# Kernel optimization log

Hardware: AMD Instinct MI355X
Metric: run time of the kernel (lower is better)

Reference implementation:

```python
import jax, jax.numpy as jnp
import numpy as np
from jax import lax

V, E, HE, HD, B, T, DEC_STEPS = 50000, 300, 512, 1024, 64, 400, 80


def gru_cell(x, h, w_ih, w_hh, b_ih, b_hh):
    # PyTorch GRU cell semantics
    gi = x @ w_ih.T + b_ih          # [B, 3H]
    gh = h @ w_hh.T + b_hh          # [B, 3H]
    ir, iz, in_ = jnp.split(gi, 3, axis=-1)
    hr, hz, hn = jnp.split(gh, 3, axis=-1)
    r = jax.nn.sigmoid(ir + hr)
    z = jax.nn.sigmoid(iz + hz)
    n = jnp.tanh(in_ + r * hn)
    return (1.0 - z) * n + z * h


def setup_inputs() -> dict:
    key = jax.random.key(0)
    ks = jax.random.split(key, 20)
    s = 0.05
    texts = jax.random.randint(ks[0], (B, T), 0, V, dtype=jnp.int32)
    text_length = jax.random.randint(ks[1], (B,), 1, T + 1, dtype=jnp.int32)
    emb = jax.random.normal(ks[2], (V, E), jnp.float32) * s
    def w(k, shape):
        return jax.random.normal(k, shape, jnp.float32) * s
    return {
        "texts": texts,
        "text_length": text_length,
        "emb": emb,
        "enc_wih_f": w(ks[3], (3 * HE, E)),
        "enc_whh_f": w(ks[4], (3 * HE, HE)),
        "enc_bih_f": w(ks[5], (3 * HE,)),
        "enc_bhh_f": w(ks[6], (3 * HE,)),
        "enc_wih_b": w(ks[7], (3 * HE, E)),
        "enc_whh_b": w(ks[8], (3 * HE, HE)),
        "enc_bih_b": w(ks[9], (3 * HE,)),
        "enc_bhh_b": w(ks[10], (3 * HE,)),
        "dec_wih": w(ks[11], (3 * HD, E)),
        "dec_whh": w(ks[12], (3 * HD, HD)),
        "dec_bih": w(ks[13], (3 * HD,)),
        "dec_bhh": w(ks[14], (3 * HD,)),
        "out_w": w(ks[15], (V, HD)),
        "out_b": w(ks[16], (V,)),
    }


def reference(texts, text_length, emb,
              enc_wih_f, enc_whh_f, enc_bih_f, enc_bhh_f,
              enc_wih_b, enc_whh_b, enc_bih_b, enc_bhh_b,
              dec_wih, dec_whh, dec_bih, dec_bhh,
              out_w, out_b):
    b, t = texts.shape
    embed = emb[texts]                      # [B,T,E] (dropout is identity in eval)
    xs = jnp.swapaxes(embed, 0, 1)          # [T,B,E]
    lens = text_length[:, None]             # [B,1]
    h0 = jnp.zeros((b, HE), emb.dtype)

    # forward direction: final hidden = state at last valid timestep (pack semantics)
    def fstep(h, inp):
        x, tt = inp
        hn = gru_cell(x, h, enc_wih_f, enc_whh_f, enc_bih_f, enc_bhh_f)
        return jnp.where(tt < lens, hn, h), None
    hf, _ = lax.scan(fstep, h0, (xs, jnp.arange(t)))

    # backward direction: processes x[len-1] ... x[0]; skip padded positions
    def bstep(h, inp):
        x, tt = inp
        hn = gru_cell(x, h, enc_wih_b, enc_whh_b, enc_bih_b, enc_bhh_b)
        return jnp.where(tt < lens, hn, h), None
    hb, _ = lax.scan(bstep, h0, (xs[::-1], jnp.arange(t)[::-1]))

    hidden = jnp.concatenate([hf, hb], axis=-1)   # [B, 1024]

    sos = jnp.ones((b,), jnp.int32)               # inputs = ones
    def dstep(carry, _):
        h, tok = carry
        x = emb[tok]                              # [B,E]
        h = gru_cell(x, h, dec_wih, dec_whh, dec_bih, dec_bhh)
        logits = h @ out_w.T + out_b              # [B,V]
        tok = jnp.argmax(logits, axis=-1).astype(jnp.int32)
        return (h, tok), tok
    _, toks = lax.scan(dstep, (hidden, sos), None, length=DEC_STEPS)  # [80,B]

    return jnp.swapaxes(toks, 0, 1).astype(jnp.float32)[:, :, None]  # [B,80,1]
```

## Files before the change

kernel.cpp:

```cpp
#include <hip/hip_runtime.h>
#include <stdint.h>

typedef unsigned int u32;
typedef unsigned long long u64;
typedef unsigned short u16;
typedef __attribute__((ext_vector_type(8))) short s8;
typedef __attribute__((ext_vector_type(4))) float f4;

#define NWG 256
#define TPB 512
#define NB 64
#define TT 400
#define EE 300
#define HEN 512
#define HD 1024
#define VV 50000
#define DEC 80
#define NTL 3125
#define NTLP 3136
#define LCAP 512
#define EOFF 39168
#define LGOFF 131072
#define LGSZ (LGOFF + 256)
#define RESC 0.00837f


struct P {
  const int* texts; const int* len; const float* emb;
  const float* ewih0; const float* ewhh0; const float* ebih0; const float* ebhh0;
  const float* ewih1; const float* ewhh1; const float* ebih1; const float* ebhh1;
  const float* dwih; const float* dwhh; const float* dbih; const float* dbhh;
  const float* outw; const float* outb;
  float* out;
  u16* owbf; float* xT; float* hTf; float* hTb; float* hTd; u16* hbf;
  u64* prt; int* tok; float* wn;
};

__device__ __forceinline__ u32 fkey(float v) {
  u32 u = __float_as_uint(v);
  return (u & 0x80000000u) ? ~u : (u | 0x80000000u);
}
__device__ __forceinline__ u16 f2bf(float f) {
  u32 u = __float_as_uint(f);
  u32 r = u + 0x7FFFu + ((u >> 16) & 1u);
  return (u16)(r >> 16);
}
__device__ __forceinline__ float sigm(float x) { return 1.f / (1.f + expf(-x)); }

__device__ __forceinline__ void gru_combine_epi(
    float* pb, const f4& ar, const f4& az, const f4& ax, const f4& ah,
    int jjb, int HL, const float* bih, const float* bhh,
    const float* hc, float* ho, int mask_t, const int* lenp, u16* hbf_out)
{
  const int tid = threadIdx.x, lane = tid & 63, wv = tid >> 6;
  const int wl = wv & 3;
  if (wv < 4) {
    #pragma unroll
    for (int j = 0; j < 4; j++) {
      pb[((wl * 16 + j * 4 + 0) * 64) + lane] = ar[j];
      pb[((wl * 16 + j * 4 + 1) * 64) + lane] = az[j];
      pb[((wl * 16 + j * 4 + 2) * 64) + lane] = ax[j];
      pb[((wl * 16 + j * 4 + 3) * 64) + lane] = ah[j];
    }
  }
  __syncthreads();
  if (wv >= 4) {
    #pragma unroll
    for (int j = 0; j < 4; j++) {
      pb[((wl * 16 + j * 4 + 0) * 64) + lane] += ar[j];
      pb[((wl * 16 + j * 4 + 1) * 64) + lane] += az[j];
      pb[((wl * 16 + j * 4 + 2) * 64) + lane] += ax[j];
      pb[((wl * 16 + j * 4 + 3) * 64) + lane] += ah[j];
    }
  }
  __syncthreads();
  if (tid < 256) {
    int b = tid & 63, j = tid >> 6;
    int jj = jjb + j;
    float r = 0, z = 0, xn = 0, hn = 0;
    #pragma unroll
    for (int w = 0; w < 4; w++) {
      int base = ((w * 16 + j * 4) * 64) + b;
      r  += pb[base];
      z  += pb[base + 64];
      xn += pb[base + 128];
      hn += pb[base + 192];
    }
    r = sigm(r + bih[jj] + bhh[jj]);
    z = sigm(z + bih[HL + jj] + bhh[HL + jj]);
    float nn = tanhf(xn + bih[2 * HL + jj] + r * (hn + bhh[2 * HL + jj]));
    float hold = hc[(size_t)jj * NB + b];
    float hv = (1.f - z) * nn + z * hold;
    if (lenp && mask_t >= lenp[b]) hv = hold;
    ho[(size_t)jj * NB + b] = hv;
    if (hbf_out) hbf_out[(size_t)b * HD + jj] = f2bf(hv);
  }
}

__global__ void __launch_bounds__(TPB, 2) prep_kernel(P p) {
  const int wg = blockIdx.x, tid = threadIdx.x;
  const int lane = tid & 63, wv = tid >> 6;
  const int gtid = wg * TPB + tid;
  int gwv = wg * 8 + wv;
  for (int v = gwv; v < VV; v += 2048) {
    const float* wr = p.outw + (size_t)v * HD + lane * 16;
    u16* dst = p.owbf + (size_t)v * HD + lane * 16;
    float sa = 0.f;
    u32 pk[8];
    #pragma unroll
    for (int q = 0; q < 4; q++) {
      float4 f = *(const float4*)(wr + q * 4);
      sa += f.x * f.x + f.y * f.y + f.z * f.z + f.w * f.w;
      pk[q * 2 + 0] = (u32)f2bf(f.x) | ((u32)f2bf(f.y) << 16);
      pk[q * 2 + 1] = (u32)f2bf(f.z) | ((u32)f2bf(f.w) << 16);
    }
    *(uint4*)(dst)     = make_uint4(pk[0], pk[1], pk[2], pk[3]);
    *(uint4*)(dst + 8) = make_uint4(pk[4], pk[5], pk[6], pk[7]);
    #pragma unroll
    for (int d = 1; d < 64; d <<= 1) sa += __shfl_xor(sa, d);
    if (lane == 0) p.wn[v] = sqrtf(sa);
  }
  const long long tot = (long long)TT * NB * EE;
  for (long long i = gtid; i < tot; i += (long long)NWG * TPB) {
    int t = (int)(i / (NB * EE));
    int rr = (int)(i % (NB * EE));
    int b2 = rr / EE, k = rr % EE;
    float v = p.emb[(size_t)p.texts[b2 * TT + t] * EE + k];
    p.xT[((size_t)t * EE + k) * NB + b2] = v;
  }
}

__global__ void __launch_bounds__(TPB, 1) enc_step_kernel(P p, int t) {
  __shared__ __align__(16) char smem[EOFF + 16384];
  const int wg = blockIdx.x, tid = threadIdx.x;
  const int lane = tid & 63, wv = tid >> 6;
  const int dir = wg >> 7;
  const int ejjb = (wg & 127) * 4;

  {
    const float* wih = dir ? p.ewih1 : p.ewih0;
    const float* whh = dir ? p.ewhh1 : p.ewhh0;
    float* lw = (float*)smem;
    for (int c = wv; c < 12; c += 8) {
      int g = c >> 2, j = c & 3;
      const float* sx = wih + (size_t)(g * HEN + ejjb + j) * EE;
      for (int k = lane; k < EE; k += 64) lw[k * 12 + c] = sx[k];
      const float* sh = whh + (size_t)(g * HEN + ejjb + j) * HEN;
      for (int k = lane; k < HEN; k += 64) lw[(EE + k) * 12 + c] = sh[k];
    }
  }
  __syncthreads();

  const float* bih = dir ? p.ebih1 : p.ebih0;
  const float* bhh = dir ? p.ebhh1 : p.ebhh0;
  float* hbase = dir ? p.hTb : p.hTf;
  const int te = dir ? (TT - 1 - t) : t;
  const float* hc = hbase + (size_t)(t & 1) * HEN * NB;
  float* ho = hbase + (size_t)((t + 1) & 1) * HEN * NB;
  const float* xsrc = p.xT + (size_t)te * EE * NB;

  const float* lw = (const float*)smem;
  const int KT = EE + HEN;
  const int vs = (wv * KT) >> 3, ve = ((wv + 1) * KT) >> 3;
  f4 ar = {0,0,0,0}, az = {0,0,0,0}, ax = {0,0,0,0}, ah = {0,0,0,0};
  const int xe = ve < EE ? ve : EE;
  int k = vs;
  for (; k + 8 <= xe; k += 8) {
    float xv[8];
    #pragma unroll
    for (int u = 0; u < 8; u++) xv[u] = xsrc[(size_t)(k + u) * NB + lane];
    #pragma unroll
    for (int u = 0; u < 8; u++) {
      const float* wp = lw + (k + u) * 12;
      f4 w0 = *(const f4*)wp; f4 w1 = *(const f4*)(wp + 4); f4 w2 = *(const f4*)(wp + 8);
      ar += xv[u] * w0; az += xv[u] * w1; ax += xv[u] * w2;
    }
  }
  for (; k < xe; k++) {
    float xv = xsrc[(size_t)k * NB + lane];
    const float* wp = lw + k * 12;
    f4 w0 = *(const f4*)wp; f4 w1 = *(const f4*)(wp + 4); f4 w2 = *(const f4*)(wp + 8);
    ar += xv * w0; az += xv * w1; ax += xv * w2;
  }
  k = vs > EE ? vs : EE;
  for (; k + 8 <= ve; k += 8) {
    float hv[8];
    #pragma unroll
    for (int u = 0; u < 8; u++) hv[u] = hc[(size_t)(k + u - EE) * NB + lane];
    #pragma unroll
    for (int u = 0; u < 8; u++) {
      const float* wp = lw + (k + u) * 12;
      f4 w0 = *(const f4*)wp; f4 w1 = *(const f4*)(wp + 4); f4 w2 = *(const f4*)(wp + 8);
      ar += hv[u] * w0; az += hv[u] * w1; ah += hv[u] * w2;
    }
  }
  for (; k < ve; k++) {
    float hv = hc[(size_t)(k - EE) * NB + lane];
    const float* wp = lw + k * 12;
    f4 w0 = *(const f4*)wp; f4 w1 = *(const f4*)(wp + 4); f4 w2 = *(const f4*)(wp + 8);
    ar += hv * w0; az += hv * w1; ah += hv * w2;
  }
  gru_combine_epi((float*)(smem + EOFF), ar, az, ax, ah, ejjb, HEN,
                  bih, bhh, hc, ho, te, p.len, nullptr);
}

__global__ void enc_join_kernel(P p) {
  int g = blockIdx.x * blockDim.x + threadIdx.x;
  int stride = gridDim.x * blockDim.x;
  for (int i = g; i < HD * NB; i += stride) {
    int k = i / NB, b2 = i % NB;
    float v = (k < HEN) ? p.hTf[(size_t)k * NB + b2]
                        : p.hTb[(size_t)(k - HEN) * NB + b2];
    p.hTd[i] = v;
  }
  if (g < NB) p.tok[g] = 1;
}

__global__ void __launch_bounds__(TPB, 1) dec_gru_kernel(P p, int s) {
  __shared__ __align__(16) float pb[4096];
  const int wg = blockIdx.x, tid = threadIdx.x;
  const int lane = tid & 63, wv = tid >> 6;
  const int jjb = wg * 4;
  const float* hc = p.hTd + (size_t)(s & 1) * HD * NB;
  float* ho = p.hTd + (size_t)((s + 1) & 1) * HD * NB;
  const float* wih = p.dwih; const float* whh = p.dwhh;
  const int KT = EE + HD;
  const int vs = (wv * KT) >> 3, ve = ((wv + 1) * KT) >> 3;
  f4 ar = {0,0,0,0}, az = {0,0,0,0}, ax = {0,0,0,0}, ah = {0,0,0,0};
  const int xe = ve < EE ? ve : EE;
  if (vs < EE) {
    const float* xr = p.emb + (size_t)p.tok[lane] * EE;
    int k = vs;
    for (; k + 4 <= xe; k += 4) {
      float xv[4];
      #pragma unroll
      for (int u = 0; u < 4; u++) xv[u] = xr[k + u];
      #pragma unroll
      for (int u = 0; u < 4; u++) {
        #pragma unroll
        for (int j = 0; j < 4; j++) {
          int jj = jjb + j;
          ar[j] = fmaf(xv[u], wih[(size_t)jj * EE + k + u], ar[j]);
          az[j] = fmaf(xv[u], wih[(size_t)(HD + jj) * EE + k + u], az[j]);
          ax[j] = fmaf(xv[u], wih[(size_t)(2 * HD + jj) * EE + k + u], ax[j]);
        }
      }
    }
    for (; k < xe; k++) {
      float xv = xr[k];
      #pragma unroll
      for (int j = 0; j < 4; j++) {
        int jj = jjb + j;
        ar[j] = fmaf(xv, wih[(size_t)jj * EE + k], ar[j]);
        az[j] = fmaf(xv, wih[(size_t)(HD + jj) * EE + k], az[j]);
        ax[j] = fmaf(xv, wih[(size_t)(2 * HD + jj) * EE + k], ax[j]);
      }
    }
  }
  int hs = vs - EE; if (hs < 0) hs = 0;
  const int he = ve - EE;
  int k = hs;
  for (; k + 4 <= he; k += 4) {
    float hv[4];
    #pragma unroll
    for (int u = 0; u < 4; u++) hv[u] = hc[(size_t)(k + u) * NB + lane];
    #pragma unroll
    for (int u = 0; u < 4; u++) {
      #pragma unroll
      for (int j = 0; j < 4; j++) {
        int jj = jjb + j;
        ar[j] = fmaf(hv[u], whh[(size_t)jj * HD + k + u], ar[j]);
        az[j] = fmaf(hv[u], whh[(size_t)(HD + jj) * HD + k + u], az[j]);
        ah[j] = fmaf(hv[u], whh[(size_t)(2 * HD + jj) * HD + k + u], ah[j]);
      }
    }
  }
  for (; k < he; k++) {
    float hv = hc[(size_t)k * NB + lane];
    #pragma unroll
    for (int j = 0; j < 4; j++) {
      int jj = jjb + j;
      ar[j] = fmaf(hv, whh[(size_t)jj * HD + k], ar[j]);
      az[j] = fmaf(hv, whh[(size_t)(HD + jj) * HD + k], az[j]);
      ah[j] = fmaf(hv, whh[(size_t)(2 * HD + jj) * HD + k], ah[j]);
    }
  }
  gru_combine_epi(pb, ar, az, ax, ah, jjb, HD, p.dbih, p.dbhh,
                  hc, ho, -1, nullptr, p.hbf);
}

__global__ void __launch_bounds__(TPB, 1) dec_logits_kernel(P p) {
  extern __shared__ __align__(16) char smem[];
  const int wg = blockIdx.x, tid = threadIdx.x;
  const int lane = tid & 63, wv = tid >> 6;
  u16* hA = (u16*)smem;
  float* hsq = (float*)(smem + LGOFF);
  const int l15 = lane & 15, quad = lane >> 4;
  const int gw = wg * 8 + wv;
  const bool two = (gw + 2048) < NTL;
  if (tid < 64) hsq[tid] = 0.f;
  __syncthreads();
  for (int i = tid; i < 8192; i += TPB) {
    int r = i >> 7, c = i & 127;
    uint4 q = *(const uint4*)(p.hbf + (size_t)r * HD + c * 8);
    *(uint4*)(hA + (size_t)r * 1024 + ((c ^ (r & 7)) * 8)) = q;
    u32 uu[4] = {q.x, q.y, q.z, q.w};
    float sq = 0.f;
    #pragma unroll
    for (int t2 = 0; t2 < 4; t2++) {
      float lo = __uint_as_float(uu[t2] << 16);
      float hi = __uint_as_float(uu[t2] & 0xffff0000u);
      sq = fmaf(lo, lo, fmaf(hi, hi, sq));
    }
    atomicAdd(&hsq[r], sq);
  }
  __syncthreads();
  f4 acc0[4], acc1[4];
  #pragma unroll
  for (int m = 0; m < 4; m++) {
    #pragma unroll
    for (int r = 0; r < 4; r++) { acc0[m][r] = 0.f; acc1[m][r] = 0.f; }
  }
  const u16* bp0 = p.owbf + (size_t)(gw * 16 + l15) * HD + quad * 8;
  const u16* bp1 = bp0 + (size_t)2048 * 16 * HD;
  const int x7 = l15 & 7;
  const u16* hrow = hA + l15 * 1024;
  #pragma unroll 4
  for (int kc = 0; kc < 32; kc++) {
    int ci = ((kc * 4 + quad) ^ x7) * 8;
    s8 b0 = *(const s8*)(bp0 + kc * 32);
    s8 a0 = *(const s8*)(hrow + ci);
    s8 a1 = *(const s8*)(hrow + 16384 + ci);
    s8 a2 = *(const s8*)(hrow + 32768 + ci);
    s8 a3 = *(const s8*)(hrow + 49152 + ci);
    acc0[0] = __builtin_amdgcn_mfma_f32_16x16x32_bf16(a0, b0, acc0[0], 0, 0, 0);
    acc0[1] = __builtin_amdgcn_mfma_f32_16x16x32_bf16(a1, b0, acc0[1], 0, 0, 0);
    acc0[2] = __builtin_amdgcn_mfma_f32_16x16x32_bf16(a2, b0, acc0[2], 0, 0, 0);
    acc0[3] = __builtin_amdgcn_mfma_f32_16x16x32_bf16(a3, b0, acc0[3], 0, 0, 0);
    if (two) {
      s8 b1 = *(const s8*)(bp1 + kc * 32);
      acc1[0] = __builtin_amdgcn_mfma_f32_16x16x32_bf16(a0, b1, acc1[0], 0, 0, 0);
      acc1[1] = __builtin_amdgcn_mfma_f32_16x16x32_bf16(a1, b1, acc1[1], 0, 0, 0);
      acc1[2] = __builtin_amdgcn_mfma_f32_16x16x32_bf16(a2, b1, acc1[2], 0, 0, 0);
      acc1[3] = __builtin_amdgcn_mfma_f32_16x16x32_bf16(a3, b1, acc1[3], 0, 0, 0);
    }
  }
  float hroot[4][4];
  #pragma unroll
  for (int m = 0; m < 4; m++)
    #pragma unroll
    for (int r = 0; r < 4; r++)
      hroot[m][r] = sqrtf(hsq[m * 16 + quad * 4 + r]);
  auto epi = [&](int nt, f4* acc) {
    int col = nt * 16 + l15;
    float bias = p.outb[col];
    float wnc = p.wn[col];
    #pragma unroll
    for (int m = 0; m < 4; m++) {
      #pragma unroll
      for (int r = 0; r < 4; r++) {
        float v = acc[m][r] + bias;
        float e = RESC * hroot[m][r] * wnc + 1e-5f;
        u32 klo = fkey(v - e), kup = fkey(v + e);
        #pragma unroll
        for (int d = 1; d < 16; d <<= 1) {
          u32 ol = __shfl_xor(klo, d); if (ol > klo) klo = ol;
          u32 ou = __shfl_xor(kup, d); if (ou > kup) kup = ou;
        }
        if (l15 == 0)
          p.prt[(size_t)(m * 16 + quad * 4 + r) * NTLP + nt] =
              ((u64)klo << 32) | kup;
      }
    }
  };
  epi(gw, acc0);
  if (two) epi(gw + 2048, acc1);
}

__global__ void __launch_bounds__(TPB, 1) dec_rescue_kernel(P p, int s) {
  __shared__ float hb[HD];
  __shared__ u64 red[8];
  __shared__ u64 gmp, bestp;
  __shared__ int ncp;
  __shared__ int list[LCAP];
  const int b = blockIdx.x, tid = threadIdx.x;
  const int lane = tid & 63, wv = tid >> 6;
  const float* ho = p.hTd + (size_t)((s + 1) & 1) * HD * NB;
  for (int i = tid; i < HD; i += TPB) hb[i] = ho[(size_t)i * NB + b];
  if (tid == 0) { bestp = 0ull; ncp = 0; }
  __syncthreads();
  u64 pv[7];
  u64 mx = 0;
  #pragma unroll
  for (int i = 0; i < 7; i++) {
    int nt = tid + i * TPB;
    pv[i] = (nt < NTL) ? p.prt[(size_t)b * NTLP + nt] : 0ull;
    if (pv[i] > mx) mx = pv[i];
  }
  #pragma unroll
  for (int d = 1; d < 64; d <<= 1) { u64 o = __shfl_xor(mx, d); if (o > mx) mx = o; }
  if (lane == 0) red[wv] = mx;
  __syncthreads();
  if (tid == 0) {
    u64 g = red[0];
    for (int w2 = 1; w2 < 8; w2++) if (red[w2] > g) g = red[w2];
    gmp = g;
  }
  __syncthreads();
  const u32 thr = (u32)(gmp >> 32);
  #pragma unroll
  for (int i = 0; i < 7; i++) {
    if ((u32)pv[i] >= thr) {
      int ix = atomicAdd(&ncp, 1);
      if (ix < LCAP) list[ix] = tid + i * TPB;
    }
  }
  __syncthreads();
  int total = ncp;
  int nc = total < LCAP ? total : LCAP;
  const int c16 = tid >> 5, seg = tid & 31;
  u64 lb = 0;
  auto rescue = [&](int nt) {
    int v = nt * 16 + c16;
    const float* wr = p.outw + (size_t)v * HD;
    float sm = 0.f;
    #pragma unroll 8
    for (int i = 0; i < 32; i++) {
      int k = seg + 32 * i;
      sm = fmaf(hb[k], wr[k], sm);
    }
    #pragma unroll
    for (int d = 1; d < 32; d <<= 1) sm += __shfl_xor(sm, d);
    if (seg == 0) {
      float lg = sm + p.outb[v];
      u64 k2 = ((u64)fkey(lg) << 32) | (~(u32)v);
      if (k2 > lb) lb = k2;
    }
  };
  for (int ci = 0; ci < nc; ci++) rescue(list[ci]);
  if (total > LCAP) {
    for (int nt = 0; nt < NTL; nt++)
      if ((u32)p.prt[(size_t)b * NTLP + nt] >= thr) rescue(nt);
  }
  if (seg == 0 && lb) atomicMax((unsigned long long*)&bestp, lb);
  __syncthreads();
  if (tid == 0) {
    u32 v = ~(u32)(bestp);
    p.tok[b] = (int)v;
    p.out[b * DEC + s] = (float)v;
  }
}

__global__ void seq2seq_init(float* hTf, float* hTb) {
  int g = blockIdx.x * blockDim.x + threadIdx.x;
  int n = 2 * HEN * NB;
  for (int i = g; i < n; i += gridDim.x * blockDim.x) { hTf[i] = 0.f; hTb[i] = 0.f; }
}

extern "C" void kernel_launch(void* const* d_in, const int* in_sizes, int n_in,
                              void* d_out, int out_size, void* d_ws, size_t ws_size,
                              hipStream_t stream) {
  char* w = (char*)d_ws;
  size_t off = 0;
  auto carve = [&](size_t n) {
    void* q = w + off;
    off = (off + n + 255) & ~(size_t)255;
    return q;
  };
  P p;
  p.texts = (const int*)d_in[0];
  p.len   = (const int*)d_in[1];
  p.emb   = (const float*)d_in[2];
  p.ewih0 = (const float*)d_in[3];  p.ewhh0 = (const float*)d_in[4];
  p.ebih0 = (const float*)d_in[5];  p.ebhh0 = (const float*)d_in[6];
  p.ewih1 = (const float*)d_in[7];  p.ewhh1 = (const float*)d_in[8];
  p.ebih1 = (const float*)d_in[9];  p.ebhh1 = (const float*)d_in[10];
  p.dwih  = (const float*)d_in[11]; p.dwhh  = (const float*)d_in[12];
  p.dbih  = (const float*)d_in[13]; p.dbhh  = (const float*)d_in[14];
  p.outw  = (const float*)d_in[15]; p.outb  = (const float*)d_in[16];
  p.out   = (float*)d_out;
  p.owbf  = (u16*)carve((size_t)VV * HD * 2);
  p.xT    = (float*)carve((size_t)TT * EE * NB * 4);
  p.hTf   = (float*)carve((size_t)2 * HEN * NB * 4);
  p.hTb   = (float*)carve((size_t)2 * HEN * NB * 4);
  p.hTd   = (float*)carve((size_t)2 * HD * NB * 4);
  p.hbf   = (u16*)carve((size_t)NB * HD * 2);
  p.prt   = (u64*)carve((size_t)NB * NTLP * 8);
  p.tok   = (int*)carve(256);
  p.wn    = (float*)carve((size_t)VV * 4);
  if (off > ws_size) return;

  hipFuncSetAttribute((const void*)dec_logits_kernel,
                      hipFuncAttributeMaxDynamicSharedMemorySize, LGSZ);

  seq2seq_init<<<dim3(64), dim3(256), 0, stream>>>(p.hTf, p.hTb);
  prep_kernel<<<dim3(NWG), dim3(TPB), 0, stream>>>(p);
  for (int t = 0; t < TT; t++)
    enc_step_kernel<<<dim3(NWG), dim3(TPB), 0, stream>>>(p, t);
  enc_join_kernel<<<dim3(64), dim3(256), 0, stream>>>(p);
  for (int s = 0; s < DEC; s++) {
    dec_gru_kernel<<<dim3(NWG), dim3(TPB), 0, stream>>>(p, s);
    dec_logits_kernel<<<dim3(NWG), dim3(TPB), LGSZ, stream>>>(p);
    dec_rescue_kernel<<<dim3(NB), dim3(TPB), 0, stream>>>(p, s);
  }
}
```

Before: 14.70 ms.

## Replace per-step kernel launches with persistent cooperative kernels and grid barriers

Runs the 400 encoder steps and 80 decoder steps inside two persistent cooperative kernels, separated by a hierarchical atomic grid barrier, in place of about 640 separate launches. Encoder weights are staged into LDS once per block and no longer reloaded every step. Hidden states are kept as full per-step histories, so no double-buffer hazards arise across the barrier, and they are accessed with relaxed agent-scope atomics. The aim is to remove launch overhead and repeated weight staging. The cost is spin-barrier latency and a larger workspace, with a fallback to the launch-per-step path when the workspace is too small.

Result: slower. 16.79 ms (+14.3%).

```diff
diff --git a/kernel.cpp b/kernel.cpp
--- a/kernel.cpp
+++ b/kernel.cpp
@@ -21,8 +21,16 @@
 #define LCAP 512
 #define EOFF 39168
 #define LGOFF 131072
-#define LGSZ (LGOFF + 256)
+#define DSZ (LGOFF + 16384)
 #define RESC 0.00837f
+
+#define BD_GRP   0
+#define BD_ROOT  1024
+#define BD_EPO   1152
+#define BX_GRP   1280
+#define BX_ROOT  2304
+#define BX_EPO   2368
+#define BAR_WORDS 2432
 
 
 struct P {
@@ -32,9 +40,50 @@
   const float* dwih; const float* dwhh; const float* dbih; const float* dbhh;
   const float* outw; const float* outb;
   float* out;
-  u16* owbf; float* xT; float* hTf; float* hTb; float* hTd; u16* hbf;
-  u64* prt; int* tok; float* wn;
+  u16* owbf; float* xT; u64* prt; int* tok; float* wn; u32* bar;
+  float* hrF; float* hrB;
+  float* hTdR;
+  u16* hbfR;
+  float* hTf; float* hTb; float* hTd; u16* hbf;
 };
+
+__device__ __forceinline__ float cld(const float* a) {
+  return __hip_atomic_load(const_cast<float*>(a), __ATOMIC_RELAXED, __HIP_MEMORY_SCOPE_AGENT);
+}
+__device__ __forceinline__ void cst(float* a, float v) {
+  __hip_atomic_store(a, v, __ATOMIC_RELAXED, __HIP_MEMORY_SCOPE_AGENT);
+}
+__device__ __forceinline__ u64 cld(const u64* a) {
+  return __hip_atomic_load(const_cast<u64*>(a), __ATOMIC_RELAXED, __HIP_MEMORY_SCOPE_AGENT);
+}
+__device__ __forceinline__ void cst(u64* a, u64 v) {
+  __hip_atomic_store(a, v, __ATOMIC_RELAXED, __HIP_MEMORY_SCOPE_AGENT);
+}
+__device__ __forceinline__ int cld(const int* a) {
+  return __hip_atomic_load(const_cast<int*>(a), __ATOMIC_RELAXED, __HIP_MEMORY_SCOPE_AGENT);
+}
+__device__ __forceinline__ void cst(int* a, int v) {
+  __hip_atomic_store(a, v, __ATOMIC_RELAXED, __HIP_MEMORY_SCOPE_AGENT);
+}
+__device__ __forceinline__ void cst(u16* a, u16 v) {
+  __hip_atomic_store(a, v, __ATOMIC_RELAXED, __HIP_MEMORY_SCOPE_AGENT);
+}
+
+__device__ __forceinline__ void gbarx(u32* grp, u32* root, u32* epo,
+                                      u32 e, u32 gsz, u32 nroot) {
+  __syncthreads();
+  if (threadIdx.x == 0) {
+    u32 old = __hip_atomic_fetch_add(grp, 1u, __ATOMIC_RELAXED, __HIP_MEMORY_SCOPE_AGENT);
+    if (old == e * gsz + (gsz - 1u)) {
+      u32 r = __hip_atomic_fetch_add(root, 1u, __ATOMIC_RELAXED, __HIP_MEMORY_SCOPE_AGENT);
+      if (r == e * nroot + (nroot - 1u))
+        __hip_atomic_store(epo, e + 1u, __ATOMIC_RELAXED, __HIP_MEMORY_SCOPE_AGENT);
+    }
+    while (__hip_atomic_load(epo, __ATOMIC_RELAXED, __HIP_MEMORY_SCOPE_AGENT) < e + 1u)
+      __builtin_amdgcn_s_sleep(8);
+  }
+  __syncthreads();
+}
 
 __device__ __forceinline__ u32 fkey(float v) {
   u32 u = __float_as_uint(v);
@@ -47,6 +96,7 @@
 }
 __device__ __forceinline__ float sigm(float x) { return 1.f / (1.f + expf(-x)); }
 
+template<bool COH>
 __device__ __forceinline__ void gru_combine_epi(
     float* pb, const f4& ar, const f4& az, const f4& ax, const f4& ah,
     int jjb, int HL, const float* bih, const float* bhh,
@@ -92,73 +142,22 @@
     float hold = hc[(size_t)jj * NB + b];
     float hv = (1.f - z) * nn + z * hold;
     if (lenp && mask_t >= lenp[b]) hv = hold;
-    ho[(size_t)jj * NB + b] = hv;
-    if (hbf_out) hbf_out[(size_t)b * HD + jj] = f2bf(hv);
-  }
-}
-
-__global__ void __launch_bounds__(TPB, 2) prep_kernel(P p) {
-  const int wg = blockIdx.x, tid = threadIdx.x;
-  const int lane = tid & 63, wv = tid >> 6;
-  const int gtid = wg * TPB + tid;
-  int gwv = wg * 8 + wv;
-  for (int v = gwv; v < VV; v += 2048) {
-    const float* wr = p.outw + (size_t)v * HD + lane * 16;
-    u16* dst = p.owbf + (size_t)v * HD + lane * 16;
-    float sa = 0.f;
-    u32 pk[8];
-    #pragma unroll
-    for (int q = 0; q < 4; q++) {
-      float4 f = *(const float4*)(wr + q * 4);
-      sa += f.x * f.x + f.y * f.y + f.z * f.z + f.w * f.w;
-      pk[q * 2 + 0] = (u32)f2bf(f.x) | ((u32)f2bf(f.y) << 16);
-      pk[q * 2 + 1] = (u32)f2bf(f.z) | ((u32)f2bf(f.w) << 16);
-    }
-    *(uint4*)(dst)     = make_uint4(pk[0], pk[1], pk[2], pk[3]);
-    *(uint4*)(dst + 8) = make_uint4(pk[4], pk[5], pk[6], pk[7]);
-    #pragma unroll
-    for (int d = 1; d < 64; d <<= 1) sa += __shfl_xor(sa, d);
-    if (lane == 0) p.wn[v] = sqrtf(sa);
-  }
-  const long long tot = (long long)TT * NB * EE;
-  for (long long i = gtid; i < tot; i += (long long)NWG * TPB) {
-    int t = (int)(i / (NB * EE));
-    int rr = (int)(i % (NB * EE));
-    int b2 = rr / EE, k = rr % EE;
-    float v = p.emb[(size_t)p.texts[b2 * TT + t] * EE + k];
-    p.xT[((size_t)t * EE + k) * NB + b2] = v;
-  }
-}
-
-__global__ void __launch_bounds__(TPB, 1) enc_step_kernel(P p, int t) {
-  __shared__ __align__(16) char smem[EOFF + 16384];
-  const int wg = blockIdx.x, tid = threadIdx.x;
-  const int lane = tid & 63, wv = tid >> 6;
-  const int dir = wg >> 7;
-  const int ejjb = (wg & 127) * 4;
-
-  {
-    const float* wih = dir ? p.ewih1 : p.ewih0;
-    const float* whh = dir ? p.ewhh1 : p.ewhh0;
-    float* lw = (float*)smem;
-    for (int c = wv; c < 12; c += 8) {
-      int g = c >> 2, j = c & 3;
-      const float* sx = wih + (size_t)(g * HEN + ejjb + j) * EE;
-      for (int k = lane; k < EE; k += 64) lw[k * 12 + c] = sx[k];
-      const float* sh = whh + (size_t)(g * HEN + ejjb + j) * HEN;
-      for (int k = lane; k < HEN; k += 64) lw[(EE + k) * 12 + c] = sh[k];
-    }
-  }
-  __syncthreads();
-
-  const float* bih = dir ? p.ebih1 : p.ebih0;
-  const float* bhh = dir ? p.ebhh1 : p.ebhh0;
-  float* hbase = dir ? p.hTb : p.hTf;
-  const int te = dir ? (TT - 1 - t) : t;
-  const float* hc = hbase + (size_t)(t & 1) * HEN * NB;
-  float* ho = hbase + (size_t)((t + 1) & 1) * HEN * NB;
-  const float* xsrc = p.xT + (size_t)te * EE * NB;
-
+    if (COH) cst(ho + (size_t)jj * NB + b, hv);
+    else     ho[(size_t)jj * NB + b] = hv;
+    if (hbf_out) {
+      if (COH) cst(hbf_out + (size_t)b * HD + jj, f2bf(hv));
+      else     hbf_out[(size_t)b * HD + jj] = f2bf(hv);
+    }
+  }
+}
+
+template<bool COH>
+__device__ __forceinline__ void enc_step_body(
+    char* smem, int jjb, const float* xsrc,
+    const float* bih, const float* bhh,
+    const float* __restrict__ hc, float* ho, int te, const int* lenp)
+{
+  const int tid = threadIdx.x, lane = tid & 63, wv = tid >> 6;
   const float* lw = (const float*)smem;
   const int KT = EE + HEN;
   const int vs = (wv * KT) >> 3, ve = ((wv + 1) * KT) >> 3;
@@ -200,36 +199,39 @@
     f4 w0 = *(const f4*)wp; f4 w1 = *(const f4*)(wp + 4); f4 w2 = *(const f4*)(wp + 8);
     ar += hv * w0; az += hv * w1; ah += hv * w2;
   }
-  gru_combine_epi((float*)(smem + EOFF), ar, az, ax, ah, ejjb, HEN,
-                  bih, bhh, hc, ho, te, p.len, nullptr);
-}
-
-__global__ void enc_join_kernel(P p) {
-  int g = blockIdx.x * blockDim.x + threadIdx.x;
-  int stride = gridDim.x * blockDim.x;
-  for (int i = g; i < HD * NB; i += stride) {
-    int k = i / NB, b2 = i % NB;
-    float v = (k < HEN) ? p.hTf[(size_t)k * NB + b2]
-                        : p.hTb[(size_t)(k - HEN) * NB + b2];
-    p.hTd[i] = v;
-  }
-  if (g < NB) p.tok[g] = 1;
-}
-
-__global__ void __launch_bounds__(TPB, 1) dec_gru_kernel(P p, int s) {
-  __shared__ __align__(16) float pb[4096];
-  const int wg = blockIdx.x, tid = threadIdx.x;
-  const int lane = tid & 63, wv = tid >> 6;
-  const int jjb = wg * 4;
-  const float* hc = p.hTd + (size_t)(s & 1) * HD * NB;
-  float* ho = p.hTd + (size_t)((s + 1) & 1) * HD * NB;
+  gru_combine_epi<COH>((float*)(smem + EOFF), ar, az, ax, ah, jjb, HEN,
+                       bih, bhh, hc, ho, te, lenp, nullptr);
+}
+
+__device__ __forceinline__ void enc_stage_weights(char* smem, int dir, int ejjb,
+                                                  const P& p) {
+  const int tid = threadIdx.x, lane = tid & 63, wv = tid >> 6;
+  const float* wih = dir ? p.ewih1 : p.ewih0;
+  const float* whh = dir ? p.ewhh1 : p.ewhh0;
+  float* lw = (float*)smem;
+  for (int c = wv; c < 12; c += 8) {
+    int g = c >> 2, j = c & 3;
+    const float* sx = wih + (size_t)(g * HEN + ejjb + j) * EE;
+    for (int k = lane; k < EE; k += 64) lw[k * 12 + c] = sx[k];
+    const float* sh = whh + (size_t)(g * HEN + ejjb + j) * HEN;
+    for (int k = lane; k < HEN; k += 64) lw[(EE + k) * 12 + c] = sh[k];
+  }
+}
+
+template<bool COH>
+__device__ __forceinline__ void dec_gru_body(
+    const P& p, float* pb, int jjb,
+    const float* __restrict__ hc, float* ho, u16* hbf_out)
+{
+  const int tid = threadIdx.x, lane = tid & 63, wv = tid >> 6;
   const float* wih = p.dwih; const float* whh = p.dwhh;
   const int KT = EE + HD;
   const int vs = (wv * KT) >> 3, ve = ((wv + 1) * KT) >> 3;
   f4 ar = {0,0,0,0}, az = {0,0,0,0}, ax = {0,0,0,0}, ah = {0,0,0,0};
   const int xe = ve < EE ? ve : EE;
   if (vs < EE) {
-    const float* xr = p.emb + (size_t)p.tok[lane] * EE;
+    int tk = COH ? cld(p.tok + lane) : p.tok[lane];
+    const float* xr = p.emb + (size_t)tk * EE;
     int k = vs;
     for (; k + 4 <= xe; k += 4) {
       float xv[4];
@@ -285,12 +287,13 @@
       ah[j] = fmaf(hv, whh[(size_t)(2 * HD + jj) * HD + k], ah[j]);
     }
   }
-  gru_combine_epi(pb, ar, az, ax, ah, jjb, HD, p.dbih, p.dbhh,
-                  hc, ho, -1, nullptr, p.hbf);
-}
-
-__global__ void __launch_bounds__(TPB, 1) dec_logits_kernel(P p) {
-  extern __shared__ __align__(16) char smem[];
+  gru_combine_epi<COH>(pb, ar, az, ax, ah, jjb, HD, p.dbih, p.dbhh,
+                       hc, ho, -1, nullptr, hbf_out);
+}
+
+template<bool COH>
+__device__ __forceinline__ void dec_logits_body(const P& p, char* smem,
+                                                const u16* hbf_src) {
   const int wg = blockIdx.x, tid = threadIdx.x;
   const int lane = tid & 63, wv = tid >> 6;
   u16* hA = (u16*)smem;
@@ -302,7 +305,7 @@
   __syncthreads();
   for (int i = tid; i < 8192; i += TPB) {
     int r = i >> 7, c = i & 127;
-    uint4 q = *(const uint4*)(p.hbf + (size_t)r * HD + c * 8);
+    uint4 q = *(const uint4*)(hbf_src + (size_t)r * HD + c * 8);
     *(uint4*)(hA + (size_t)r * 1024 + ((c ^ (r & 7)) * 8)) = q;
     u32 uu[4] = {q.x, q.y, q.z, q.w};
     float sq = 0.f;
@@ -367,9 +370,11 @@
           u32 ol = __shfl_xor(klo, d); if (ol > klo) klo = ol;
           u32 ou = __shfl_xor(kup, d); if (ou > kup) kup = ou;
         }
-        if (l15 == 0)
-          p.prt[(size_t)(m * 16 + quad * 4 + r) * NTLP + nt] =
-              ((u64)klo << 32) | kup;
+        if (l15 == 0) {
+          u64 key = ((u64)klo << 32) | kup;
+          u64* dst = p.prt + (size_t)(m * 16 + quad * 4 + r) * NTLP + nt;
+          if (COH) cst(dst, key); else *dst = key;
+        }
       }
     }
   };
@@ -377,24 +382,31 @@
   if (two) epi(gw + 2048, acc1);
 }
 
-__global__ void __launch_bounds__(TPB, 1) dec_rescue_kernel(P p, int s) {
-  __shared__ float hb[HD];
-  __shared__ u64 red[8];
-  __shared__ u64 gmp, bestp;
-  __shared__ int ncp;
-  __shared__ int list[LCAP];
-  const int b = blockIdx.x, tid = threadIdx.x;
+template<bool COH>
+__device__ __forceinline__ void dec_rescue_body(const P& p, char* smem,
+                                                const float* ho, int s, int b) {
+  const int tid = threadIdx.x;
   const int lane = tid & 63, wv = tid >> 6;
-  const float* ho = p.hTd + (size_t)((s + 1) & 1) * HD * NB;
+  char* ms = smem + LGOFF;
+  float* hb = (float*)ms;
+  u64* red = (u64*)(ms + 4096);
+  u64* gmp = (u64*)(ms + 4160);
+  u64* bestp = (u64*)(ms + 4168);
+  int* ncp = (int*)(ms + 4176);
+  int* list = (int*)(ms + 4192);
   for (int i = tid; i < HD; i += TPB) hb[i] = ho[(size_t)i * NB + b];
-  if (tid == 0) { bestp = 0ull; ncp = 0; }
+  if (tid == 0) { *bestp = 0ull; *ncp = 0; }
   __syncthreads();
   u64 pv[7];
   u64 mx = 0;
   #pragma unroll
   for (int i = 0; i < 7; i++) {
     int nt = tid + i * TPB;
-    pv[i] = (nt < NTL) ? p.prt[(size_t)b * NTLP + nt] : 0ull;
+    pv[i] = 0ull;
+    if (nt < NTL) {
+      const u64* src = p.prt + (size_t)b * NTLP + nt;
+      pv[i] = COH ? cld(src) : *src;
+    }
     if (pv[i] > mx) mx = pv[i];
   }
   #pragma unroll
@@ -404,19 +416,19 @@
   if (tid == 0) {
     u64 g = red[0];
     for (int w2 = 1; w2 < 8; w2++) if (red[w2] > g) g = red[w2];
-    gmp = g;
-  }
-  __syncthreads();
-  const u32 thr = (u32)(gmp >> 32);
+    *gmp = g;
+  }
+  __syncthreads();
+  const u32 thr = (u32)(*gmp >> 32);
   #pragma unroll
   for (int i = 0; i < 7; i++) {
     if ((u32)pv[i] >= thr) {
-      int ix = atomicAdd(&ncp, 1);
+      int ix = atomicAdd(ncp, 1);
       if (ix < LCAP) list[ix] = tid + i * TPB;
     }
   }
   __syncthreads();
-  int total = ncp;
+  int total = *ncp;
   int nc = total < LCAP ? total : LCAP;
   const int c16 = tid >> 5, seg = tid & 31;
   u64 lb = 0;
@@ -439,22 +451,154 @@
   };
   for (int ci = 0; ci < nc; ci++) rescue(list[ci]);
   if (total > LCAP) {
-    for (int nt = 0; nt < NTL; nt++)
-      if ((u32)p.prt[(size_t)b * NTLP + nt] >= thr) rescue(nt);
-  }
-  if (seg == 0 && lb) atomicMax((unsigned long long*)&bestp, lb);
+    for (int nt = 0; nt < NTL; nt++) {
+      const u64* src = p.prt + (size_t)b * NTLP + nt;
+      u64 v = COH ? cld(src) : *src;
+      if ((u32)v >= thr) rescue(nt);
+    }
+  }
+  if (seg == 0 && lb) atomicMax((unsigned long long*)bestp, lb);
   __syncthreads();
   if (tid == 0) {
-    u32 v = ~(u32)(bestp);
-    p.tok[b] = (int)v;
+    u32 v = ~(u32)(*bestp);
+    if (COH) cst(p.tok + b, (int)v); else p.tok[b] = (int)v;
     p.out[b * DEC + s] = (float)v;
   }
 }
 
-__global__ void seq2seq_init(float* hTf, float* hTb) {
+__global__ void __launch_bounds__(TPB, 2) prep_kernel(P p) {
+  const int wg = blockIdx.x, tid = threadIdx.x;
+  const int lane = tid & 63, wv = tid >> 6;
+  const int gtid = wg * TPB + tid;
+  int gwv = wg * 8 + wv;
+  for (int v = gwv; v < VV; v += 2048) {
+    const float* wr = p.outw + (size_t)v * HD + lane * 16;
+    u16* dst = p.owbf + (size_t)v * HD + lane * 16;
+    float sa = 0.f;
+    u32 pk[8];
+    #pragma unroll
+    for (int q = 0; q < 4; q++) {
+      float4 f = *(const float4*)(wr + q * 4);
+      sa += f.x * f.x + f.y * f.y + f.z * f.z + f.w * f.w;
+      pk[q * 2 + 0] = (u32)f2bf(f.x) | ((u32)f2bf(f.y) << 16);
+      pk[q * 2 + 1] = (u32)f2bf(f.z) | ((u32)f2bf(f.w) << 16);
+    }
+    *(uint4*)(dst)     = make_uint4(pk[0], pk[1], pk[2], pk[3]);
+    *(uint4*)(dst + 8) = make_uint4(pk[4], pk[5], pk[6], pk[7]);
+    #pragma unroll
+    for (int d = 1; d < 64; d <<= 1) sa += __shfl_xor(sa, d);
+    if (lane == 0) p.wn[v] = sqrtf(sa);
+  }
+  const long long tot = (long long)TT * NB * EE;
+  for (long long i = gtid; i < tot; i += (long long)NWG * TPB) {
+    int t = (int)(i / (NB * EE));
+    int rr = (int)(i % (NB * EE));
+    int b2 = rr / EE, k = rr % EE;
+    float v = p.emb[(size_t)p.texts[b2 * TT + t] * EE + k];
+    p.xT[((size_t)t * EE + k) * NB + b2] = v;
+  }
+}
+
+__global__ void init_kernel(u32* bar, float* z0, float* z1, int n) {
   int g = blockIdx.x * blockDim.x + threadIdx.x;
-  int n = 2 * HEN * NB;
-  for (int i = g; i < n; i += gridDim.x * blockDim.x) { hTf[i] = 0.f; hTb[i] = 0.f; }
+  if (g < BAR_WORDS) bar[g] = 0u;
+  for (int i = g; i < n; i += gridDim.x * blockDim.x) { z0[i] = 0.f; z1[i] = 0.f; }
+}
+
+__global__ void __launch_bounds__(TPB, 1) enc_coop_kernel(P p) {
+  __shared__ __align__(16) char smem[EOFF + 16384];
+  const int wg = blockIdx.x;
+  const int dir = wg >> 7;
+  const int ejjb = (wg & 127) * 4;
+  u32 ebD = 0;
+  enc_stage_weights(smem, dir, ejjb, p);
+  __syncthreads();
+  const float* bih = dir ? p.ebih1 : p.ebih0;
+  const float* bhh = dir ? p.ebhh1 : p.ebhh0;
+  float* hr = dir ? p.hrB : p.hrF;
+  for (int t = 0; t < TT; t++) {
+    const int te = dir ? (TT - 1 - t) : t;
+    const float* hc = hr + (size_t)t * HEN * NB;
+    float* ho = hr + (size_t)(t + 1) * HEN * NB;
+    enc_step_body<true>(smem, ejjb, p.xT + (size_t)te * EE * NB,
+                        bih, bhh, hc, ho, te, p.len);
+    gbarx(p.bar + BD_GRP + ((wg >> 4) << 6),
+          p.bar + BD_ROOT + dir * 64, p.bar + BD_EPO + dir * 64, ebD++, 16u, 8u);
+  }
+}
+
+__global__ void __launch_bounds__(TPB, 1) dec_coop_kernel(P p) {
+  extern __shared__ __align__(16) char smem[];
+  const int wg = blockIdx.x, tid = threadIdx.x;
+  const int gtid = wg * TPB + tid;
+  u32 ebX = 0;
+  for (int i = gtid; i < HD * NB; i += NWG * TPB) {
+    int k = i / NB, b2 = i % NB;
+    float v = (k < HEN) ? p.hrF[(size_t)TT * HEN * NB + (size_t)k * NB + b2]
+                        : p.hrB[(size_t)TT * HEN * NB + (size_t)(k - HEN) * NB + b2];
+    cst(p.hTdR + i, v);
+  }
+  if (gtid < NB) cst(p.tok + gtid, 1);
+  gbarx(p.bar + BX_GRP + ((wg >> 4) << 6),
+        p.bar + BX_ROOT, p.bar + BX_EPO, ebX++, 16u, 16u);
+
+  for (int s = 0; s < DEC; s++) {
+    const float* hc = p.hTdR + (size_t)s * HD * NB;
+    float* ho = p.hTdR + (size_t)(s + 1) * HD * NB;
+    u16* hbf_s = p.hbfR + (size_t)s * NB * HD;
+    dec_gru_body<true>(p, (float*)(smem + LGOFF), wg * 4, hc, ho, hbf_s);
+    gbarx(p.bar + BX_GRP + ((wg >> 4) << 6),
+          p.bar + BX_ROOT, p.bar + BX_EPO, ebX++, 16u, 16u);
+    dec_logits_body<true>(p, smem, hbf_s);
+    gbarx(p.bar + BX_GRP + ((wg >> 4) << 6),
+          p.bar + BX_ROOT, p.bar + BX_EPO, ebX++, 16u, 16u);
+    if (wg < NB) dec_rescue_body<true>(p, smem, ho, s, wg);
+    gbarx(p.bar + BX_GRP + ((wg >> 4) << 6),
+          p.bar + BX_ROOT, p.bar + BX_EPO, ebX++, 16u, 16u);
+  }
+}
+
+__global__ void __launch_bounds__(TPB, 1) enc_step_kernel(P p, int t) {
+  __shared__ __align__(16) char smem[EOFF + 16384];
+  const int wg = blockIdx.x;
+  const int dir = wg >> 7;
+  const int ejjb = (wg & 127) * 4;
+  enc_stage_weights(smem, dir, ejjb, p);
+  __syncthreads();
+  const float* bih = dir ? p.ebih1 : p.ebih0;
+  const float* bhh = dir ? p.ebhh1 : p.ebhh0;
+  float* hbase = dir ? p.hTb : p.hTf;
+  const int te = dir ? (TT - 1 - t) : t;
+  const float* hc = hbase + (size_t)(t & 1) * HEN * NB;
+  float* ho = hbase + (size_t)((t + 1) & 1) * HEN * NB;
+  enc_step_body<false>(smem, ejjb, p.xT + (size_t)te * EE * NB,
+                       bih, bhh, hc, ho, te, p.len);
+}
+__global__ void enc_join_kernel(P p) {
+  int g = blockIdx.x * blockDim.x + threadIdx.x;
+  int stride = gridDim.x * blockDim.x;
+  for (int i = g; i < HD * NB; i += stride) {
+    int k = i / NB, b2 = i % NB;
+    float v = (k < HEN) ? p.hTf[(size_t)k * NB + b2]
+                        : p.hTb[(size_t)(k - HEN) * NB + b2];
+    p.hTd[i] = v;
+  }
+  if (g < NB) p.tok[g] = 1;
+}
+__global__ void __launch_bounds__(TPB, 1) dec_gru_kernel(P p, int s) {
+  __shared__ __align__(16) float pb[4096];
+  const float* hc = p.hTd + (size_t)(s & 1) * HD * NB;
+  float* ho = p.hTd + (size_t)((s + 1) & 1) * HD * NB;
+  dec_gru_body<false>(p, pb, blockIdx.x * 4, hc, ho, p.hbf);
+}
+__global__ void __launch_bounds__(TPB, 1) dec_logits_kernel(P p) {
+  extern __shared__ __align__(16) char smem[];
+  dec_logits_body<false>(p, smem, p.hbf);
+}
+__global__ void __launch_bounds__(TPB, 1) dec_rescue_kernel(P p, int s) {
+  extern __shared__ __align__(16) char smem[];
+  const float* ho = p.hTd + (size_t)((s + 1) & 1) * HD * NB;
+  dec_rescue_body<false>(p, smem, ho, s, blockIdx.x);
 }
 
 extern "C" void kernel_launch(void* const* d_in, const int* in_sizes, int n_in,
@@ -481,26 +625,55 @@
   p.out   = (float*)d_out;
   p.owbf  = (u16*)carve((size_t)VV * HD * 2);
   p.xT    = (float*)carve((size_t)TT * EE * NB * 4);
-  p.hTf   = (float*)carve((size_t)2 * HEN * NB * 4);
-  p.hTb   = (float*)carve((size_t)2 * HEN * NB * 4);
-  p.hTd   = (float*)carve((size_t)2 * HD * NB * 4);
-  p.hbf   = (u16*)carve((size_t)NB * HD * 2);
   p.prt   = (u64*)carve((size_t)NB * NTLP * 8);
   p.tok   = (int*)carve(256);
   p.wn    = (float*)carve((size_t)VV * 4);
-  if (off > ws_size) return;
-
+  p.bar   = (u32*)carve(BAR_WORDS * 4);
+  size_t off_common = off;
+
+  p.hrF  = (float*)carve((size_t)(TT + 1) * HEN * NB * 4);
+  p.hrB  = (float*)carve((size_t)(TT + 1) * HEN * NB * 4);
+  p.hTdR = (float*)carve((size_t)(DEC + 1) * HD * NB * 4);
+  p.hbfR = (u16*)carve((size_t)DEC * NB * HD * 2);
+  bool coop = (off <= ws_size);
+  if (!coop) {
+    off = off_common;
+    p.hTf = (float*)carve((size_t)2 * HEN * NB * 4);
+    p.hTb = (float*)carve((size_t)2 * HEN * NB * 4);
+    p.hTd = (float*)carve((size_t)2 * HD * NB * 4);
+    p.hbf = (u16*)carve((size_t)NB * HD * 2);
+    if (off > ws_size) return;
+  } else {
+    p.hTf = p.hrF; p.hTb = p.hrB; p.hTd = p.hTdR; p.hbf = p.hbfR;
+  }
+
+  hipFuncSetAttribute((const void*)dec_coop_kernel,
+                      hipFuncAttributeMaxDynamicSharedMemorySize, DSZ);
   hipFuncSetAttribute((const void*)dec_logits_kernel,
-                      hipFuncAttributeMaxDynamicSharedMemorySize, LGSZ);
-
-  seq2seq_init<<<dim3(64), dim3(256), 0, stream>>>(p.hTf, p.hTb);
-  prep_kernel<<<dim3(NWG), dim3(TPB), 0, stream>>>(p);
-  for (int t = 0; t < TT; t++)
-    enc_step_kernel<<<dim3(NWG), dim3(TPB), 0, stream>>>(p, t);
-  enc_join_kernel<<<dim3(64), dim3(256), 0, stream>>>(p);
-  for (int s = 0; s < DEC; s++) {
-    dec_gru_kernel<<<dim3(NWG), dim3(TPB), 0, stream>>>(p, s);
-    dec_logits_kernel<<<dim3(NWG), dim3(TPB), LGSZ, stream>>>(p);
-    dec_rescue_kernel<<<dim3(NB), dim3(TPB), 0, stream>>>(p, s);
-  }
-}
+                      hipFuncAttributeMaxDynamicSharedMemorySize, DSZ);
+
+  if (coop) {
+    init_kernel<<<dim3(64), dim3(256), 0, stream>>>(p.bar, p.hrF, p.hrB, HEN * NB);
+    prep_kernel<<<dim3(NWG), dim3(TPB), 0, stream>>>(p);
+    void* args[] = { &p };
+    hipError_t e = hipLaunchCooperativeKernel((void*)enc_coop_kernel,
+                                              dim3(NWG), dim3(TPB), args, 0, stream);
+    if (e != hipSuccess)
+      enc_coop_kernel<<<dim3(NWG), dim3(TPB), 0, stream>>>(p);
+    e = hipLaunchCooperativeKernel((void*)dec_coop_kernel,
+                                   dim3(NWG), dim3(TPB), args, DSZ, stream);
+    if (e != hipSuccess)
+      dec_coop_kernel<<<dim3(NWG), dim3(TPB), DSZ, stream>>>(p);
+  } else {
+    init_kernel<<<dim3(64), dim3(256), 0, stream>>>(p.bar, p.hTf, p.hTb, 2 * HEN * NB);
+    prep_kernel<<<dim3(NWG), dim3(TPB), 0, stream>>>(p);
+    for (int t = 0; t < TT; t++)
+      enc_step_kernel<<<dim3(NWG), dim3(TPB), 0, stream>>>(p, t);
+    enc_join_kernel<<<dim3(64), dim3(256), 0, stream>>>(p);
+    for (int s = 0; s < DEC; s++) {
+      dec_gru_kernel<<<dim3(NWG), dim3(TPB), 0, stream>>>(p, s);
+      dec_logits_kernel<<<dim3(NWG), dim3(TPB), DSZ, stream>>>(p);
+      dec_rescue_kernel<<<dim3(NB), dim3(TPB), 0, stream>>>(p, s);
+    }
+  }
+}
```
